# Kernel optimization log

Hardware: AMD Instinct MI355X
Metric: run time of the kernel (lower is better)

The kernel has to match this reference:

```python
import jax, jax.numpy as jnp
import numpy as np

K = 9  # kernel_size (knn neighbors, loop=True -> self included)

def setup_inputs() -> dict:
    key = jax.random.key(0)
    k1, k2, k3 = jax.random.split(key, 3)
    B, C, H, W = 8, 64, 32, 32
    OUT = 64
    x = jax.random.normal(k1, (B, C, H, W), dtype=jnp.float32)
    # SAGEConv params: lin_l (neighbor aggregate, with bias), lin_r (root, no bias)
    s = 1.0 / np.sqrt(C)
    W_l = jax.random.uniform(k2, (OUT, C), minval=-s, maxval=s, dtype=jnp.float32)
    b_l = jnp.zeros((OUT,), dtype=jnp.float32)
    W_r = jax.random.uniform(k3, (OUT, C), minval=-s, maxval=s, dtype=jnp.float32)
    return {"x": x, "W_l": W_l, "b_l": b_l, "W_r": W_r}

def _knn_mean(x_f, batches):
    # squared-euclidean pairwise distances [N, N], masked across batches
    sq = jnp.sum(x_f * x_f, axis=-1)
    dist = sq[:, None] + sq[None, :] - 2.0 * (x_f @ x_f.T)
    cross = batches[:, None] != batches[None, :]
    dist = jnp.where(cross, jnp.inf, dist)
    neg, idx = jax.lax.top_k(-dist, K)          # k nearest (self included, dist 0)
    valid = (neg != -jnp.inf).astype(x_f.dtype)  # handle degenerate last-batch node
    nbr = x_f[idx] * valid[..., None]            # [N, K, C]
    return nbr.sum(axis=1) / valid.sum(axis=1, keepdims=True)

def reference(x, W_l, b_l, W_r):
    B, C, H, Wd = x.shape
    N = B * H * Wd
    x_f = x.transpose(0, 2, 3, 1).reshape(N, C)  # flat_nodes: [B*H*W, C]
    # torch.linspace(0, B, steps=N).to(int64): truncation of i*B/(N-1)
    batches = jnp.linspace(0.0, float(B), N).astype(jnp.int32)
    mean_nbr = _knn_mean(x_f, batches)
    # SAGEConv: lin_l(mean_j x_j) + lin_r(x_i)
    return mean_nbr @ W_l.T + b_l + x_f @ W_r.T
```

## Files before the change

kernel.cpp:

```cpp
#include <hip/hip_runtime.h>
#include <cstdint>
#include <cstddef>


__global__ __launch_bounds__(256, 2) void k_dist(const float* __restrict__ x,
                                                 float* __restrict__ xf,
                                                 float* __restrict__ D) {
  __shared__ float4 As4[32 * 33];
  __shared__ float4 Bs4[32 * 33];
  __shared__ float sqA[128];
  __shared__ float sqB[128];
  int cx = blockIdx.x;
  int i0 = (int)blockIdx.y << 7;
  int s = (i0 >= 7168) ? 7168 : (i0 & ~1023);
  int j0 = s + (cx << 7);
  const float* xA = x + (((size_t)(i0 >> 10)) << 16) + (i0 & 1023);
  const float* xB = x + (((size_t)(j0 >> 10)) << 16) + (j0 & 1023);
  int t = threadIdx.x;
  int tx = t & 15, ty = t >> 4;

  float acc[8][8];
#pragma unroll
  for (int r = 0; r < 8; ++r)
#pragma unroll
    for (int c = 0; c < 8; ++c) acc[r][c] = 0.f;

#pragma unroll 1
  for (int pass = 0; pass < 2; ++pass) {
    if (pass) __syncthreads();
    int c0 = pass << 5;
#pragma unroll
    for (int i = 0; i < 4; ++i) {
      int u = t + (i << 8);
      int c = u >> 5, m4 = u & 31;
      As4[c * 33 + m4] = *(const float4*)&xA[((size_t)(c0 + c) << 10) + (m4 << 2)];
      Bs4[c * 33 + m4] = *(const float4*)&xB[((size_t)(c0 + c) << 10) + (m4 << 2)];
    }
    __syncthreads();
    {
      int m = t & 127;
      const float* base = (t < 128) ? (const float*)As4 : (const float*)Bs4;
      float p = 0.f;
#pragma unroll
      for (int c = 0; c < 32; ++c) {
        float v = base[(c * 33 + (m >> 2)) * 4 + (m & 3)];
        p = fmaf(v, v, p);
      }
      float* dst = (t < 128) ? sqA : sqB;
      if (pass == 0) dst[m] = p; else dst[m] += p;
    }
    if (cx == 0) {
#pragma unroll
      for (int i = 0; i < 16; ++i) {
        int u = t + (i << 8);
        int c = u & 31, m = u >> 5;
        xf[((size_t)(i0 + m) << 6) + c0 + c] =
            ((const float*)As4)[(c * 33 + (m >> 2)) * 4 + (m & 3)];
      }
    }
#pragma unroll 4
    for (int k = 0; k < 32; ++k) {
      float4 a0 = As4[k * 33 + ty];
      float4 a1 = As4[k * 33 + 16 + ty];
      float4 b0 = Bs4[k * 33 + tx];
      float4 b1 = Bs4[k * 33 + 16 + tx];
      float av[8] = {a0.x, a0.y, a0.z, a0.w, a1.x, a1.y, a1.z, a1.w};
      float bv[8] = {b0.x, b0.y, b0.z, b0.w, b1.x, b1.y, b1.z, b1.w};
#pragma unroll
      for (int r = 0; r < 8; ++r)
#pragma unroll
        for (int c = 0; c < 8; ++c)
          acc[r][c] = fmaf(av[r], bv[c], acc[r][c]);
    }
  }
  __syncthreads();

  int rloc[8], cloc[8];
#pragma unroll
  for (int r = 0; r < 4; ++r) { rloc[r] = (ty << 2) + r; rloc[4 + r] = 64 + (ty << 2) + r; }
#pragma unroll
  for (int c = 0; c < 4; ++c) { cloc[c] = (tx << 2) + c; cloc[4 + c] = 64 + (tx << 2) + c; }
  float sqi[8], sqj[8];
#pragma unroll
  for (int r = 0; r < 8; ++r) sqi[r] = sqA[rloc[r]];
#pragma unroll
  for (int c = 0; c < 8; ++c) sqj[c] = sqB[cloc[c]];
#pragma unroll
  for (int r = 0; r < 8; ++r) {
    size_t rb = ((size_t)(i0 + rloc[r]) << 10) + (cx << 7);
    float4 o0, o1;
    o0.x = sqi[r] + sqj[0] - 2.f * acc[r][0];
    o0.y = sqi[r] + sqj[1] - 2.f * acc[r][1];
    o0.z = sqi[r] + sqj[2] - 2.f * acc[r][2];
    o0.w = sqi[r] + sqj[3] - 2.f * acc[r][3];
    o1.x = sqi[r] + sqj[4] - 2.f * acc[r][4];
    o1.y = sqi[r] + sqj[5] - 2.f * acc[r][5];
    o1.z = sqi[r] + sqj[6] - 2.f * acc[r][6];
    o1.w = sqi[r] + sqj[7] - 2.f * acc[r][7];
    *(float4*)&D[rb + (tx << 2)] = o0;
    *(float4*)&D[rb + 64 + (tx << 2)] = o1;
  }
}

__global__ __launch_bounds__(256, 2) void k_selout(const float* __restrict__ D,
                                                   const float* __restrict__ xf,
                                                   const float* __restrict__ Wl,
                                                   const float* __restrict__ bl,
                                                   const float* __restrict__ Wr,
                                                   float* __restrict__ out) {
  __shared__ float WsL[64][65];
  __shared__ float WsR[64][65];
  int t = threadIdx.x;
#pragma unroll
  for (int i = 0; i < 16; ++i) {
    int lin = t + (i << 8);
    WsL[lin >> 6][lin & 63] = Wl[lin];
    WsR[lin >> 6][lin & 63] = Wr[lin];
  }
  __syncthreads();
  int lane = t & 63;
  float wl[64], wr[64];
#pragma unroll
  for (int c = 0; c < 64; ++c) { wl[c] = WsL[lane][c]; wr[c] = WsR[lane][c]; }
  float bias = bl[lane];
  int w = t >> 6;
  int n0 = ((int)blockIdx.x << 4) + (w << 2);

  unsigned j9[4][9];
#pragma unroll
  for (int r = 0; r < 4; ++r) {
    int n = n0 + r;
    if (n == 8191) { j9[r][0] = 8191u; continue; }
    int s = (n >= 7168) ? 7168 : (n & ~1023);
    bool mlast = (n >= 7168);
    const float* drow = D + ((size_t)n << 10);
    unsigned long long cand[16];
#pragma unroll
    for (int q = 0; q < 4; ++q) {
      float4 v = *(const float4*)&drow[(lane << 4) + (q << 2)];
      float vv[4] = {v.x, v.y, v.z, v.w};
#pragma unroll
      for (int e = 0; e < 4; ++e) {
        int slot = (q << 2) + e;
        unsigned u = __float_as_uint(vv[e]);
        u = (u & 0x80000000u) ? ~u : (u | 0x80000000u);
        cand[slot] = ((unsigned long long)u << 32) | (unsigned)((lane << 4) + slot);
      }
    }
    if (mlast && lane == 63) cand[15] = ~0ull;
    unsigned long long m1 = cand[0], m2 = cand[1];
    if (m2 < m1) { unsigned long long tt = m1; m1 = m2; m2 = tt; }
#pragma unroll
    for (int q = 2; q < 16; ++q) {
      unsigned long long c = cand[q];
      unsigned long long lo = (c < m1) ? c : m1;
      unsigned long long hi = (c < m1) ? m1 : c;
      m2 = (hi < m2) ? hi : m2;
      m1 = lo;
    }
    unsigned long long lm = m1;
    unsigned rmask = 0;
    bool stale = false;
#pragma unroll
    for (int kk = 0; kk < 9; ++kk) {
      unsigned long long g = lm;
#pragma unroll
      for (int off = 32; off; off >>= 1) {
        unsigned ghi = __shfl_xor((unsigned)(g >> 32), off, 64);
        unsigned glo = __shfl_xor((unsigned)g, off, 64);
        unsigned long long o = ((unsigned long long)ghi << 32) | glo;
        g = (o < g) ? o : g;
      }
      j9[r][kk] = (unsigned)s + ((unsigned)g & 1023u);
      if (lm == g) {
        rmask |= 1u << (unsigned)(g & 15u);
        if (!stale) { lm = m2; stale = true; }
        else {
          unsigned long long best = ~0ull;
#pragma unroll
          for (int q = 0; q < 16; ++q) {
            bool alive = ((rmask >> q) & 1u) == 0u;
            unsigned long long c = cand[q];
            best = (alive && c < best) ? c : best;
          }
          lm = best;
        }
      }
    }
  }

  float ms[4], xr[4];
#pragma unroll
  for (int r = 0; r < 4; ++r) {
    int n = n0 + r;
    int cnt = (n == 8191) ? 1 : 9;
    float msum = 0.f;
    for (int k = 0; k < cnt; ++k)
      msum += xf[((size_t)j9[r][k] << 6) + lane];
    ms[r] = msum / (float)cnt;
    xr[r] = xf[((size_t)n << 6) + lane];
  }
  float accL[4] = {0.f, 0.f, 0.f, 0.f};
  float accR[4] = {0.f, 0.f, 0.f, 0.f};
#pragma unroll
  for (int c = 0; c < 64; ++c) {
#pragma unroll
    for (int r = 0; r < 4; ++r) {
      float mc = __int_as_float(__builtin_amdgcn_readlane(__float_as_int(ms[r]), c));
      float xc = __int_as_float(__builtin_amdgcn_readlane(__float_as_int(xr[r]), c));
      accL[r] = fmaf(mc, wl[c], accL[r]);
      accR[r] = fmaf(xc, wr[c], accR[r]);
    }
  }
#pragma unroll
  for (int r = 0; r < 4; ++r)
    out[((size_t)(n0 + r) << 6) + lane] = accL[r] + accR[r] + bias;
}

extern "C" void kernel_launch(void* const* d_in, const int* in_sizes, int n_in,
                              void* d_out, int out_size, void* d_ws, size_t ws_size,
                              hipStream_t stream) {
  const float* x  = (const float*)d_in[0];
  const float* Wl = (const float*)d_in[1];
  const float* bl = (const float*)d_in[2];
  const float* Wr = (const float*)d_in[3];
  float* out = (float*)d_out;

  char* ws = (char*)d_ws;
  float* xf = (float*)(ws);
  float* D  = (float*)(ws + 2097152);

  k_dist<<<dim3(8, 64), 256, 0, stream>>>(x, xf, D);
  k_selout<<<512, 256, 0, stream>>>(D, xf, Wl, bl, Wr, out);
}
```

Before: 107.2 us.

## Fuse partial top-9 selection into distance kernel, merge partials in output kernel

The distance kernel no longer writes the full 8192x1024 distance matrix. Each 128-column tile now does a per-row top-9 selection with 16-lane shuffle reductions and writes 9 packed 64-bit keys per row per tile. The output kernel merges the 72 candidates per row with a short wavefront reduction and then does the same mean and linear layers. This removes the 32MB distance write and read, at the cost of more selection work and shuffles inside the GEMM kernel.

```diff
diff --git a/kernel.cpp b/kernel.cpp
--- a/kernel.cpp
+++ b/kernel.cpp
@@ -3,9 +3,18 @@
 #include <cstddef>
 
 
-__global__ __launch_bounds__(256, 2) void k_dist(const float* __restrict__ x,
-                                                 float* __restrict__ xf,
-                                                 float* __restrict__ D) {
+__device__ __forceinline__ unsigned mono32(float d) {
+  unsigned u = __float_as_uint(d);
+  return (u & 0x80000000u) ? ~u : (u | 0x80000000u);
+}
+
+__device__ __forceinline__ float rdlane(float v, int src) {
+  return __int_as_float(__builtin_amdgcn_readlane(__float_as_int(v), src));
+}
+
+__global__ __launch_bounds__(256, 2) void k_dist_topk(const float* __restrict__ x,
+                                                      float* __restrict__ xf,
+                                                      unsigned long long* __restrict__ part) {
   __shared__ float4 As4[32 * 33];
   __shared__ float4 Bs4[32 * 33];
   __shared__ float sqA[128];
@@ -85,29 +94,72 @@
   for (int r = 0; r < 8; ++r) sqi[r] = sqA[rloc[r]];
 #pragma unroll
   for (int c = 0; c < 8; ++c) sqj[c] = sqB[cloc[c]];
+  bool excl = (s == 7168) && (cx == 7);
+
 #pragma unroll
   for (int r = 0; r < 8; ++r) {
-    size_t rb = ((size_t)(i0 + rloc[r]) << 10) + (cx << 7);
-    float4 o0, o1;
-    o0.x = sqi[r] + sqj[0] - 2.f * acc[r][0];
-    o0.y = sqi[r] + sqj[1] - 2.f * acc[r][1];
-    o0.z = sqi[r] + sqj[2] - 2.f * acc[r][2];
-    o0.w = sqi[r] + sqj[3] - 2.f * acc[r][3];
-    o1.x = sqi[r] + sqj[4] - 2.f * acc[r][4];
-    o1.y = sqi[r] + sqj[5] - 2.f * acc[r][5];
-    o1.z = sqi[r] + sqj[6] - 2.f * acc[r][6];
-    o1.w = sqi[r] + sqj[7] - 2.f * acc[r][7];
-    *(float4*)&D[rb + (tx << 2)] = o0;
-    *(float4*)&D[rb + 64 + (tx << 2)] = o1;
-  }
-}
-
-__global__ __launch_bounds__(256, 2) void k_selout(const float* __restrict__ D,
-                                                   const float* __restrict__ xf,
-                                                   const float* __restrict__ Wl,
-                                                   const float* __restrict__ bl,
-                                                   const float* __restrict__ Wr,
-                                                   float* __restrict__ out) {
+    int row = i0 + rloc[r];
+    unsigned long long k8[8];
+#pragma unroll
+    for (int c = 0; c < 8; ++c) {
+      float dv = sqi[r] + sqj[c] - 2.f * acc[r][c];
+      unsigned jj = (unsigned)((cx << 7) + cloc[c]);
+      unsigned long long key = ((unsigned long long)mono32(dv) << 32) | jj;
+      if (excl && cloc[c] == 127) key = ~0ull;
+      k8[c] = key;
+    }
+    unsigned long long m1 = k8[0], m2 = k8[1];
+    int s1 = 0, s2 = 1;
+    if (m2 < m1) { unsigned long long tt = m1; m1 = m2; m2 = tt; s1 = 1; s2 = 0; }
+#pragma unroll
+    for (int c = 2; c < 8; ++c) {
+      unsigned long long kc = k8[c];
+      bool lt1 = kc < m1, lt2 = kc < m2;
+      m2 = lt1 ? m1 : (lt2 ? kc : m2);
+      s2 = lt1 ? s1 : (lt2 ? c : s2);
+      m1 = lt1 ? kc : m1;
+      s1 = lt1 ? c : s1;
+    }
+    unsigned long long lm = m1;
+    int lms = s1;
+    unsigned rmask = 0;
+    bool stale = false;
+#pragma unroll
+    for (int kk = 0; kk < 9; ++kk) {
+      unsigned long long g = lm;
+#pragma unroll
+      for (int off = 8; off; off >>= 1) {
+        unsigned hi = (unsigned)__shfl_xor((int)(unsigned)(g >> 32), off, 64);
+        unsigned lo = (unsigned)__shfl_xor((int)(unsigned)g, off, 64);
+        unsigned long long o = ((unsigned long long)hi << 32) | lo;
+        g = (o < g) ? o : g;
+      }
+      if (tx == kk) part[((size_t)((row << 3) | cx)) * 9 + kk] = g;
+      if (lm == g) {
+        rmask |= 1u << lms;
+        if (!stale) { lm = m2; lms = s2; stale = true; }
+        else {
+          unsigned long long bd = ~0ull; int bs = 0;
+#pragma unroll
+          for (int c = 0; c < 8; ++c) {
+            bool alive = ((rmask >> c) & 1u) == 0u;
+            bool take = alive && (k8[c] < bd);
+            bd = take ? k8[c] : bd;
+            bs = take ? c : bs;
+          }
+          lm = bd; lms = bs;
+        }
+      }
+    }
+  }
+}
+
+__global__ __launch_bounds__(256, 2) void k_merge_out(const unsigned long long* __restrict__ part,
+                                                      const float* __restrict__ xf,
+                                                      const float* __restrict__ Wl,
+                                                      const float* __restrict__ bl,
+                                                      const float* __restrict__ Wr,
+                                                      float* __restrict__ out) {
   __shared__ float WsL[64][65];
   __shared__ float WsR[64][65];
   int t = threadIdx.x;
@@ -130,62 +182,29 @@
 #pragma unroll
   for (int r = 0; r < 4; ++r) {
     int n = n0 + r;
-    if (n == 8191) { j9[r][0] = 8191u; continue; }
+    if (n == 8191) {
+#pragma unroll
+      for (int kk = 0; kk < 9; ++kk) j9[r][kk] = 8191u;
+      continue;
+    }
     int s = (n >= 7168) ? 7168 : (n & ~1023);
-    bool mlast = (n >= 7168);
-    const float* drow = D + ((size_t)n << 10);
-    unsigned long long cand[16];
-#pragma unroll
-    for (int q = 0; q < 4; ++q) {
-      float4 v = *(const float4*)&drow[(lane << 4) + (q << 2)];
-      float vv[4] = {v.x, v.y, v.z, v.w};
-#pragma unroll
-      for (int e = 0; e < 4; ++e) {
-        int slot = (q << 2) + e;
-        unsigned u = __float_as_uint(vv[e]);
-        u = (u & 0x80000000u) ? ~u : (u | 0x80000000u);
-        cand[slot] = ((unsigned long long)u << 32) | (unsigned)((lane << 4) + slot);
-      }
-    }
-    if (mlast && lane == 63) cand[15] = ~0ull;
-    unsigned long long m1 = cand[0], m2 = cand[1];
-    if (m2 < m1) { unsigned long long tt = m1; m1 = m2; m2 = tt; }
-#pragma unroll
-    for (int q = 2; q < 16; ++q) {
-      unsigned long long c = cand[q];
-      unsigned long long lo = (c < m1) ? c : m1;
-      unsigned long long hi = (c < m1) ? m1 : c;
-      m2 = (hi < m2) ? hi : m2;
-      m1 = lo;
-    }
-    unsigned long long lm = m1;
-    unsigned rmask = 0;
-    bool stale = false;
+    const unsigned long long* p72 = part + (size_t)n * 72;
+    unsigned long long a = p72[lane];
+    unsigned long long b2 = (lane < 8) ? p72[64 + lane] : ~0ull;
+    unsigned long long lm = (a < b2) ? a : b2;
+    unsigned long long nx = (a < b2) ? b2 : a;
 #pragma unroll
     for (int kk = 0; kk < 9; ++kk) {
       unsigned long long g = lm;
 #pragma unroll
       for (int off = 32; off; off >>= 1) {
-        unsigned ghi = __shfl_xor((unsigned)(g >> 32), off, 64);
-        unsigned glo = __shfl_xor((unsigned)g, off, 64);
-        unsigned long long o = ((unsigned long long)ghi << 32) | glo;
+        unsigned hi = (unsigned)__shfl_xor((int)(unsigned)(g >> 32), off, 64);
+        unsigned lo = (unsigned)__shfl_xor((int)(unsigned)g, off, 64);
+        unsigned long long o = ((unsigned long long)hi << 32) | lo;
         g = (o < g) ? o : g;
       }
-      j9[r][kk] = (unsigned)s + ((unsigned)g & 1023u);
-      if (lm == g) {
-        rmask |= 1u << (unsigned)(g & 15u);
-        if (!stale) { lm = m2; stale = true; }
-        else {
-          unsigned long long best = ~0ull;
-#pragma unroll
-          for (int q = 0; q < 16; ++q) {
-            bool alive = ((rmask >> q) & 1u) == 0u;
-            unsigned long long c = cand[q];
-            best = (alive && c < best) ? c : best;
-          }
-          lm = best;
-        }
-      }
+      j9[r][kk] = (unsigned)s + (unsigned)(g & 1023u);
+      if (lm == g) { lm = nx; nx = ~0ull; }
     }
   }
 
@@ -193,11 +212,11 @@
 #pragma unroll
   for (int r = 0; r < 4; ++r) {
     int n = n0 + r;
-    int cnt = (n == 8191) ? 1 : 9;
     float msum = 0.f;
-    for (int k = 0; k < cnt; ++k)
+#pragma unroll
+    for (int k = 0; k < 9; ++k)
       msum += xf[((size_t)j9[r][k] << 6) + lane];
-    ms[r] = msum / (float)cnt;
+    ms[r] = msum / 9.0f;
     xr[r] = xf[((size_t)n << 6) + lane];
   }
   float accL[4] = {0.f, 0.f, 0.f, 0.f};
@@ -206,8 +225,8 @@
   for (int c = 0; c < 64; ++c) {
 #pragma unroll
     for (int r = 0; r < 4; ++r) {
-      float mc = __int_as_float(__builtin_amdgcn_readlane(__float_as_int(ms[r]), c));
-      float xc = __int_as_float(__builtin_amdgcn_readlane(__float_as_int(xr[r]), c));
+      float mc = rdlane(ms[r], c);
+      float xc = rdlane(xr[r], c);
       accL[r] = fmaf(mc, wl[c], accL[r]);
       accR[r] = fmaf(xc, wr[c], accR[r]);
     }
@@ -228,8 +247,9 @@
 
   char* ws = (char*)d_ws;
   float* xf = (float*)(ws);
-  float* D  = (float*)(ws + 2097152);
-
-  k_dist<<<dim3(8, 64), 256, 0, stream>>>(x, xf, D);
-  k_selout<<<512, 256, 0, stream>>>(D, xf, Wl, bl, Wr, out);
-}
+  unsigned long long* part =
+      (unsigned long long*)(ws + 2097152);
+
+  k_dist_topk<<<dim3(8, 64), 256, 0, stream>>>(x, xf, part);
+  k_merge_out<<<512, 256, 0, stream>>>(part, xf, Wl, bl, Wr, out);
+}
```

Result: slower. 121.0 us (+12.9%).
